# Kernel tuning notes

Measured on AMD Instinct MI355X. Metric: run time of the kernel, lower is better.

## Reference

```python
import jax, jax.numpy as jnp
import numpy as np

B, G, GS = 1024, 2000, 25   # batch, num gene groups, group size
H1, H2, C = 1024, 512, 10
EPS = 1e-5


def _xavier(key, shape, fan_in, fan_out):
    lim = np.sqrt(6.0 / (fan_in + fan_out))
    return jax.random.uniform(key, shape, jnp.float32, -lim, lim)


def setup_inputs() -> dict:
    key = jax.random.key(0)
    ks = jax.random.split(key, 8)
    x = jax.random.normal(ks[0], (B, G * GS), jnp.float32)
    # per-group Linear(GS, 1) weights stacked -> block-diagonal grouped GEMM
    gene_w = _xavier(ks[1], (G, GS), GS, 1)
    gene_b = jnp.zeros((G,), jnp.float32)
    W1 = _xavier(ks[2], (G, H1), G, H1)
    b1 = jnp.zeros((H1,), jnp.float32)
    W2 = _xavier(ks[3], (H1, H2), H1, H2)
    b2 = jnp.zeros((H2,), jnp.float32)
    Wout = _xavier(ks[4], (H2, C), H2, C)
    bout = jnp.zeros((C,), jnp.float32)
    Wres = _xavier(ks[5], (G, C), G, C)
    bres = jnp.zeros((C,), jnp.float32)
    gamma1 = jnp.ones((H1,), jnp.float32); beta1 = jnp.zeros((H1,), jnp.float32)
    gamma2 = jnp.ones((H2,), jnp.float32); beta2 = jnp.zeros((H2,), jnp.float32)
    return dict(x=x, gene_w=gene_w, gene_b=gene_b, W1=W1, b1=b1,
                gamma1=gamma1, beta1=beta1, W2=W2, b2=b2,
                gamma2=gamma2, beta2=beta2, Wout=Wout, bout=bout,
                Wres=Wres, bres=bres)


def _batch_norm(h, gamma, beta):
    # training-mode BatchNorm1d: biased batch statistics over axis 0
    mu = jnp.mean(h, axis=0)
    var = jnp.mean(jnp.square(h - mu), axis=0)
    return gamma * (h - mu) * jax.lax.rsqrt(var + EPS) + beta


def reference(x, gene_w, gene_b, W1, b1, gamma1, beta1, W2, b2,
              gamma2, beta2, Wout, bout, Wres, bres):
    # fused replacement for the per-group Linear(GS,1)+ReLU loop + cat
    xg = x.reshape(B, G, GS)
    g = jax.nn.relu(jnp.einsum('bgk,gk->bg', xg, gene_w) + gene_b)  # [B, G]
    h1 = jax.nn.relu(_batch_norm(g @ W1 + b1, gamma1, beta1))       # [B, H1]
    h2 = jax.nn.relu(_batch_norm(h1 @ W2 + b2, gamma2, beta2))      # [B, H2]
    x_main = h2 @ Wout + bout                                       # [B, C]
    x_res = g @ Wres + bres                                         # [B, C]
    return jax.nn.softmax(x_main + x_res, axis=1)
```

## Files before the change

kernel.cpp:

```cpp
#include <hip/hip_runtime.h>
#include <math.h>

#define NB   1024
#define NG   2000
#define NGS  25
#define KP   2048
#define NH1  1024
#define NH2  512
#define NC   10
#define EPSV 1e-5f
#define GPB  200

typedef __attribute__((ext_vector_type(8))) __bf16 bf16x8;
typedef __attribute__((ext_vector_type(4))) float f32x4;
typedef __attribute__((ext_vector_type(8))) unsigned short u16x8;
typedef __attribute__((ext_vector_type(4))) unsigned short u16x4;

__device__ __forceinline__ unsigned short f2bf(float f) {
  union { float f; unsigned u; } v; v.f = f;
  return (unsigned short)((v.u + 0x7fffu + ((v.u >> 16) & 1u)) >> 16);
}
__device__ __forceinline__ float bf2f(unsigned short b) {
  union { unsigned u; float f; } v; v.u = ((unsigned)b) << 16;
  return v.f;
}

__global__ __launch_bounds__(256) void gene_kernel(
    const float* __restrict__ x, const float* __restrict__ gw,
    const float* __restrict__ gb, unsigned short* __restrict__ g_bf) {
  __shared__ float xs[GPB * NGS];
  int b = blockIdx.x;
  int blk = blockIdx.y;
  const float4* src = (const float4*)(x + (size_t)b * (NG * NGS) + blk * (GPB * NGS));
  float4* dst = (float4*)xs;
  for (int i = threadIdx.x; i < (GPB * NGS) / 4; i += 256) dst[i] = src[i];
  __syncthreads();
  int j = threadIdx.x;
  if (j < GPB) {
    int gi = blk * GPB + j;
    const float* wp = gw + gi * NGS;
    const float* xp = xs + j * NGS;
    float acc = 0.f;
#pragma unroll
    for (int k = 0; k < NGS; ++k) acc = fmaf(xp[k], wp[k], acc);
    acc += gb[gi];
    g_bf[(size_t)b * KP + gi] = f2bf(fmaxf(acc, 0.f));
  } else if (blk == (NG / GPB - 1) && j < GPB + (KP - NG)) {
    g_bf[(size_t)b * KP + NG + (j - GPB)] = 0;
  }
}

__global__ __launch_bounds__(256) void convT_kernel(
    const float* __restrict__ src, unsigned short* __restrict__ dst,
    int K, int N, int Kpad) {
  __shared__ unsigned short ts[64][72];
  int k0 = blockIdx.x * 64, n0 = blockIdx.y * 64;
  int t = threadIdx.x;
  int c4 = (t & 15) * 4;
  int r  = t >> 4;
  for (int rr = r; rr < 64; rr += 16) {
    int k = k0 + rr;
    float4 v = make_float4(0.f, 0.f, 0.f, 0.f);
    if (k < K) v = *(const float4*)&src[(size_t)k * N + n0 + c4];
    ts[rr][c4 + 0] = f2bf(v.x); ts[rr][c4 + 1] = f2bf(v.y);
    ts[rr][c4 + 2] = f2bf(v.z); ts[rr][c4 + 3] = f2bf(v.w);
  }
  __syncthreads();
  int rr8 = (t & 7) * 8;
  int cc  = t >> 3;
  for (int c = cc; c < 64; c += 32) {
    u16x8 val;
#pragma unroll
    for (int i = 0; i < 8; ++i) val[i] = ts[rr8 + i][c];
    *(u16x8*)&dst[(size_t)(n0 + c) * Kpad + k0 + rr8] = val;
  }
}

__global__ __launch_bounds__(256) void gemm_bf16(
    const unsigned short* __restrict__ A,
    const unsigned short* __restrict__ Bt,
    float* __restrict__ C, int M, int N, int Kp) {
  __shared__ unsigned short As[64][72];
  __shared__ unsigned short Bs[64][72];
  int t = threadIdx.x;
  int m0 = blockIdx.y * 64, n0 = blockIdx.x * 64;
  int wave = t >> 6, lane = t & 63;
  int wm = (wave >> 1) * 32, wn = (wave & 1) * 32;
  int fm = lane & 15;
  int fk = (lane >> 4) * 8;

  int srow = t >> 3;
  int skc  = (t & 7) * 8;

  f32x4 acc[2][2];
#pragma unroll
  for (int i = 0; i < 2; ++i)
#pragma unroll
    for (int j = 0; j < 2; ++j) acc[i][j] = (f32x4){0.f, 0.f, 0.f, 0.f};

  const unsigned short* Ap = A + (size_t)(m0 + srow) * Kp + skc;
  const unsigned short* Bp = Bt + (size_t)(n0 + srow) * Kp + skc;
  size_t rstep = 32 * (size_t)Kp;

  u16x8 pa0 = *(const u16x8*)(Ap);
  u16x8 pa1 = *(const u16x8*)(Ap + rstep);
  u16x8 pb0 = *(const u16x8*)(Bp);
  u16x8 pb1 = *(const u16x8*)(Bp + rstep);

  for (int k0 = 0; k0 < Kp; k0 += 64) {
    *(u16x8*)&As[srow][skc]      = pa0;
    *(u16x8*)&As[srow + 32][skc] = pa1;
    *(u16x8*)&Bs[srow][skc]      = pb0;
    *(u16x8*)&Bs[srow + 32][skc] = pb1;
    __syncthreads();
    if (k0 + 64 < Kp) {
      pa0 = *(const u16x8*)(Ap + k0 + 64);
      pa1 = *(const u16x8*)(Ap + k0 + 64 + rstep);
      pb0 = *(const u16x8*)(Bp + k0 + 64);
      pb1 = *(const u16x8*)(Bp + k0 + 64 + rstep);
    }
#pragma unroll
    for (int s = 0; s < 2; ++s) {
      bf16x8 af[2], bfr[2];
      af[0]  = *(const bf16x8*)&As[wm + fm][s * 32 + fk];
      af[1]  = *(const bf16x8*)&As[wm + 16 + fm][s * 32 + fk];
      bfr[0] = *(const bf16x8*)&Bs[wn + fm][s * 32 + fk];
      bfr[1] = *(const bf16x8*)&Bs[wn + 16 + fm][s * 32 + fk];
#pragma unroll
      for (int i = 0; i < 2; ++i)
#pragma unroll
        for (int j = 0; j < 2; ++j)
          acc[i][j] = __builtin_amdgcn_mfma_f32_16x16x32_bf16(
              af[i], bfr[j], acc[i][j], 0, 0, 0);
    }
    __syncthreads();
  }

  int crow = (lane >> 4) * 4;
  int ccol = lane & 15;
#pragma unroll
  for (int i = 0; i < 2; ++i)
#pragma unroll
    for (int j = 0; j < 2; ++j)
#pragma unroll
      for (int r = 0; r < 4; ++r) {
        int m = m0 + wm + i * 16 + crow + r;
        int n = n0 + wn + j * 16 + ccol;
        C[(size_t)m * N + n] = acc[i][j][r];
      }
}

__global__ __launch_bounds__(256) void bn_stats(
    const float* __restrict__ t, float* __restrict__ sum,
    float* __restrict__ sq, int N) {
  int c  = blockIdx.x * blockDim.x + threadIdx.x;
  int r0 = blockIdx.y * 64;
  float s = 0.f, ss = 0.f;
  for (int r = r0; r < r0 + 64; ++r) {
    float v = t[(size_t)r * N + c];
    s += v;
    ss = fmaf(v, v, ss);
  }
  atomicAdd(&sum[c], s);
  atomicAdd(&sq[c], ss);
}

__global__ __launch_bounds__(256) void bn_apply_bf16(
    const float* __restrict__ t, unsigned short* __restrict__ o,
    const float* __restrict__ sum, const float* __restrict__ sq,
    const float* __restrict__ gamma, const float* __restrict__ beta,
    int nmask) {
  int idx = (blockIdx.x * 256 + threadIdx.x) * 4;
  float4 v = *(const float4*)&t[idx];
  float vv[4] = {v.x, v.y, v.z, v.w};
  u16x4 ov;
#pragma unroll
  for (int i = 0; i < 4; ++i) {
    int c = (idx + i) & nmask;
    float mu  = sum[c] * (1.f / NB);
    float var = sq[c] * (1.f / NB) - mu * mu;
    float h = (vv[i] - mu) * rsqrtf(var + EPSV);
    ov[i] = f2bf(fmaxf(fmaf(gamma[c], h, beta[c]), 0.f));
  }
  *(u16x4*)&o[idx] = ov;
}

__global__ __launch_bounds__(256) void bn_apply_f32(
    float* __restrict__ t, const float* __restrict__ sum,
    const float* __restrict__ sq, const float* __restrict__ gamma,
    const float* __restrict__ beta, int nmask) {
  int idx = (blockIdx.x * 256 + threadIdx.x) * 4;
  float4 v = *(const float4*)&t[idx];
  float vv[4] = {v.x, v.y, v.z, v.w};
#pragma unroll
  for (int i = 0; i < 4; ++i) {
    int c = (idx + i) & nmask;
    float mu  = sum[c] * (1.f / NB);
    float var = sq[c] * (1.f / NB) - mu * mu;
    float h = (vv[i] - mu) * rsqrtf(var + EPSV);
    vv[i] = fmaxf(fmaf(gamma[c], h, beta[c]), 0.f);
  }
  *(float4*)&t[idx] = make_float4(vv[0], vv[1], vv[2], vv[3]);
}

__global__ __launch_bounds__(256) void final_kernel(
    const float* __restrict__ h2, const unsigned short* __restrict__ g_bf,
    const float* __restrict__ Wout, const float* __restrict__ bout,
    const float* __restrict__ Wres, const float* __restrict__ bres,
    float* __restrict__ out) {
  int b = blockIdx.x;
  int t = threadIdx.x;
  float acc[NC] = {};

  if (t < NH2 / 4) {
    float4 hv = *(const float4*)&h2[(size_t)b * NH2 + t * 4];
    float hr[4] = {hv.x, hv.y, hv.z, hv.w};
    const float4* wp = (const float4*)&Wout[t * 4 * NC];
    float w[40];
#pragma unroll
    for (int q = 0; q < 10; ++q) {
      float4 wv = wp[q];
      w[q * 4] = wv.x; w[q * 4 + 1] = wv.y; w[q * 4 + 2] = wv.z; w[q * 4 + 3] = wv.w;
    }
#pragma unroll
    for (int r = 0; r < 4; ++r)
#pragma unroll
      for (int c = 0; c < NC; ++c) acc[c] = fmaf(hr[r], w[r * NC + c], acc[c]);
  }

  for (int u = t; u < NG / 4; u += 256) {
    u16x4 gv = *(const u16x4*)&g_bf[(size_t)b * KP + u * 4];
    float gr[4] = {bf2f(gv[0]), bf2f(gv[1]), bf2f(gv[2]), bf2f(gv[3])};
    const float4* wp = (const float4*)&Wres[u * 4 * NC];
    float w[40];
#pragma unroll
    for (int q = 0; q < 10; ++q) {
      float4 wv = wp[q];
      w[q * 4] = wv.x; w[q * 4 + 1] = wv.y; w[q * 4 + 2] = wv.z; w[q * 4 + 3] = wv.w;
    }
#pragma unroll
    for (int r = 0; r < 4; ++r)
#pragma unroll
      for (int c = 0; c < NC; ++c) acc[c] = fmaf(gr[r], w[r * NC + c], acc[c]);
  }

  __shared__ float red[4][NC];
  __shared__ float logits[NC];
  int lane = t & 63, wave = t >> 6;
#pragma unroll
  for (int c = 0; c < NC; ++c) {
    float v = acc[c];
    for (int off = 32; off > 0; off >>= 1) v += __shfl_down(v, off, 64);
    if (lane == 0) red[wave][c] = v;
  }
  __syncthreads();
  if (t < NC)
    logits[t] = red[0][t] + red[1][t] + red[2][t] + red[3][t] + bout[t] + bres[t];
  __syncthreads();
  if (t == 0) {
    float mx = logits[0];
#pragma unroll
    for (int c = 1; c < NC; ++c) mx = fmaxf(mx, logits[c]);
    float e[NC], s = 0.f;
#pragma unroll
    for (int c = 0; c < NC; ++c) { e[c] = expf(logits[c] - mx); s += e[c]; }
    float inv = 1.f / s;
#pragma unroll
    for (int c = 0; c < NC; ++c) out[(size_t)b * NC + c] = e[c] * inv;
  }
}

extern "C" void kernel_launch(void* const* d_in, const int* in_sizes, int n_in,
                              void* d_out, int out_size, void* d_ws, size_t ws_size,
                              hipStream_t stream) {
  const float* x      = (const float*)d_in[0];
  const float* gw     = (const float*)d_in[1];
  const float* gb     = (const float*)d_in[2];
  const float* W1     = (const float*)d_in[3];
  const float* gamma1 = (const float*)d_in[5];
  const float* beta1  = (const float*)d_in[6];
  const float* W2     = (const float*)d_in[7];
  const float* gamma2 = (const float*)d_in[9];
  const float* beta2  = (const float*)d_in[10];
  const float* Wout   = (const float*)d_in[11];
  const float* bout   = (const float*)d_in[12];
  const float* Wres   = (const float*)d_in[13];
  const float* bres   = (const float*)d_in[14];
  float* out = (float*)d_out;

  char* p = (char*)d_ws;
  unsigned short* g_bf  = (unsigned short*)p; p += (size_t)NB * KP * 2;
  unsigned short* W1bT  = (unsigned short*)p; p += (size_t)NH1 * KP * 2;
  unsigned short* W2bT  = (unsigned short*)p; p += (size_t)NH2 * NH1 * 2;
  float* t1  = (float*)p; p += (size_t)NB * NH1 * 4;
  unsigned short* t1b = (unsigned short*)p; p += (size_t)NB * NH1 * 2;
  float* t2  = (float*)p; p += (size_t)NB * NH2 * 4;
  float* stats = (float*)p;
  float* sum1 = stats, *sq1 = stats + 1024, *sum2 = stats + 2048, *sq2 = stats + 2560;

  hipMemsetAsync(stats, 0, 3072 * sizeof(float), stream);

  convT_kernel<<<dim3(KP / 64, NH1 / 64), 256, 0, stream>>>(W1, W1bT, NG, NH1, KP);
  convT_kernel<<<dim3(NH1 / 64, NH2 / 64), 256, 0, stream>>>(W2, W2bT, NH1, NH2, NH1);

  gene_kernel<<<dim3(NB, NG / GPB), 256, 0, stream>>>(x, gw, gb, g_bf);

  gemm_bf16<<<dim3(NH1 / 64, NB / 64), 256, 0, stream>>>(g_bf, W1bT, t1, NB, NH1, KP);
  bn_stats<<<dim3(NH1 / 256, 16), 256, 0, stream>>>(t1, sum1, sq1, NH1);
  bn_apply_bf16<<<(NB * NH1 / 4) / 256, 256, 0, stream>>>(t1, t1b, sum1, sq1,
                                                          gamma1, beta1, NH1 - 1);

  gemm_bf16<<<dim3(NH2 / 64, NB / 64), 256, 0, stream>>>(t1b, W2bT, t2, NB, NH2, NH1);
  bn_stats<<<dim3(NH2 / 256, 16), 256, 0, stream>>>(t2, sum2, sq2, NH2);
  bn_apply_f32<<<(NB * NH2 / 4) / 256, 256, 0, stream>>>(t2, sum2, sq2,
                                                         gamma2, beta2, NH2 - 1);

  final_kernel<<<NB, 256, 0, stream>>>(t2, g_bf, Wout, bout, Wres, bres, out);
}
```

Baseline: 386.0 us.

## Fuse BatchNorm stats into GEMM epilogues and BN apply into consumer loads

BatchNorm column statistics are now accumulated in the GEMM epilogues via wave shuffles and atomics, which removes the separate bn_stats passes. BN1 apply plus ReLU plus the bf16 cast moves into the A-tile load of the second GEMM, and BN2 apply moves into the final kernel. The two weight-transpose launches are merged into one grid. This removes several full-tensor read/write passes and kernel launches, at the cost of extra per-tile normalization math and fp32 A loads in GEMM2.

```diff
diff --git a/kernel.cpp b/kernel.cpp
--- a/kernel.cpp
+++ b/kernel.cpp
@@ -50,9 +50,15 @@
   }
 }
 
-__global__ __launch_bounds__(256) void convT_kernel(
-    const float* __restrict__ src, unsigned short* __restrict__ dst,
-    int K, int N, int Kpad) {
+__global__ __launch_bounds__(256) void convT_dual(
+    const float* __restrict__ W1, unsigned short* __restrict__ W1bT,
+    const float* __restrict__ W2, unsigned short* __restrict__ W2bT) {
+  const float* src; unsigned short* dst; int K, N, Kpad;
+  if (blockIdx.z == 0) { src = W1; dst = W1bT; K = NG; N = NH1; Kpad = KP; }
+  else {
+    src = W2; dst = W2bT; K = NH1; N = NH2; Kpad = NH1;
+    if (blockIdx.x >= NH1 / 64 || blockIdx.y >= NH2 / 64) return;
+  }
   __shared__ unsigned short ts[64][72];
   int k0 = blockIdx.x * 64, n0 = blockIdx.y * 64;
   int t = threadIdx.x;
@@ -76,21 +82,19 @@
   }
 }
 
-__global__ __launch_bounds__(256) void gemm_bf16(
+__global__ __launch_bounds__(256) void gemm1_kernel(
     const unsigned short* __restrict__ A,
     const unsigned short* __restrict__ Bt,
-    float* __restrict__ C, int M, int N, int Kp) {
+    float* __restrict__ C, float* __restrict__ sum, float* __restrict__ sq,
+    int M, int N, int Kp) {
   __shared__ unsigned short As[64][72];
   __shared__ unsigned short Bs[64][72];
   int t = threadIdx.x;
   int m0 = blockIdx.y * 64, n0 = blockIdx.x * 64;
   int wave = t >> 6, lane = t & 63;
   int wm = (wave >> 1) * 32, wn = (wave & 1) * 32;
-  int fm = lane & 15;
-  int fk = (lane >> 4) * 8;
-
-  int srow = t >> 3;
-  int skc  = (t & 7) * 8;
+  int fm = lane & 15, fk = (lane >> 4) * 8;
+  int srow = t >> 3, skc = (t & 7) * 8;
 
   f32x4 acc[2][2];
 #pragma unroll
@@ -136,75 +140,142 @@
     __syncthreads();
   }
 
-  int crow = (lane >> 4) * 4;
-  int ccol = lane & 15;
-#pragma unroll
-  for (int i = 0; i < 2; ++i)
-#pragma unroll
-    for (int j = 0; j < 2; ++j)
+  int crow = (lane >> 4) * 4, ccol = lane & 15;
+#pragma unroll
+  for (int j = 0; j < 2; ++j) {
+    float s = 0.f, ss = 0.f;
+#pragma unroll
+    for (int i = 0; i < 2; ++i)
 #pragma unroll
       for (int r = 0; r < 4; ++r) {
+        float v = acc[i][j][r];
         int m = m0 + wm + i * 16 + crow + r;
         int n = n0 + wn + j * 16 + ccol;
-        C[(size_t)m * N + n] = acc[i][j][r];
+        C[(size_t)m * N + n] = v;
+        s += v;
+        ss = fmaf(v, v, ss);
       }
-}
-
-__global__ __launch_bounds__(256) void bn_stats(
-    const float* __restrict__ t, float* __restrict__ sum,
-    float* __restrict__ sq, int N) {
-  int c  = blockIdx.x * blockDim.x + threadIdx.x;
-  int r0 = blockIdx.y * 64;
-  float s = 0.f, ss = 0.f;
-  for (int r = r0; r < r0 + 64; ++r) {
-    float v = t[(size_t)r * N + c];
-    s += v;
-    ss = fmaf(v, v, ss);
-  }
-  atomicAdd(&sum[c], s);
-  atomicAdd(&sq[c], ss);
-}
-
-__global__ __launch_bounds__(256) void bn_apply_bf16(
-    const float* __restrict__ t, unsigned short* __restrict__ o,
-    const float* __restrict__ sum, const float* __restrict__ sq,
-    const float* __restrict__ gamma, const float* __restrict__ beta,
-    int nmask) {
-  int idx = (blockIdx.x * 256 + threadIdx.x) * 4;
-  float4 v = *(const float4*)&t[idx];
-  float vv[4] = {v.x, v.y, v.z, v.w};
-  u16x4 ov;
-#pragma unroll
-  for (int i = 0; i < 4; ++i) {
-    int c = (idx + i) & nmask;
-    float mu  = sum[c] * (1.f / NB);
-    float var = sq[c] * (1.f / NB) - mu * mu;
-    float h = (vv[i] - mu) * rsqrtf(var + EPSV);
-    ov[i] = f2bf(fmaxf(fmaf(gamma[c], h, beta[c]), 0.f));
-  }
-  *(u16x4*)&o[idx] = ov;
-}
-
-__global__ __launch_bounds__(256) void bn_apply_f32(
-    float* __restrict__ t, const float* __restrict__ sum,
-    const float* __restrict__ sq, const float* __restrict__ gamma,
-    const float* __restrict__ beta, int nmask) {
-  int idx = (blockIdx.x * 256 + threadIdx.x) * 4;
-  float4 v = *(const float4*)&t[idx];
-  float vv[4] = {v.x, v.y, v.z, v.w};
-#pragma unroll
-  for (int i = 0; i < 4; ++i) {
-    int c = (idx + i) & nmask;
-    float mu  = sum[c] * (1.f / NB);
-    float var = sq[c] * (1.f / NB) - mu * mu;
-    float h = (vv[i] - mu) * rsqrtf(var + EPSV);
-    vv[i] = fmaxf(fmaf(gamma[c], h, beta[c]), 0.f);
-  }
-  *(float4*)&t[idx] = make_float4(vv[0], vv[1], vv[2], vv[3]);
+    s  += __shfl_down(s, 32, 64);  s  += __shfl_down(s, 16, 64);
+    ss += __shfl_down(ss, 32, 64); ss += __shfl_down(ss, 16, 64);
+    if (lane < 16) {
+      atomicAdd(&sum[n0 + wn + j * 16 + lane], s);
+      atomicAdd(&sq[n0 + wn + j * 16 + lane], ss);
+    }
+  }
+}
+
+__global__ __launch_bounds__(256) void gemm2_kernel(
+    const float* __restrict__ A,
+    const unsigned short* __restrict__ Bt,
+    float* __restrict__ C, const float* __restrict__ sum1,
+    const float* __restrict__ sq1, const float* __restrict__ gam1,
+    const float* __restrict__ bet1, float* __restrict__ sum2,
+    float* __restrict__ sq2, int M, int N, int Kp) {
+  __shared__ unsigned short As[64][72];
+  __shared__ unsigned short Bs[64][72];
+  int t = threadIdx.x;
+  int m0 = blockIdx.y * 64, n0 = blockIdx.x * 64;
+  int wave = t >> 6, lane = t & 63;
+  int wm = (wave >> 1) * 32, wn = (wave & 1) * 32;
+  int fm = lane & 15, fk = (lane >> 4) * 8;
+  int srow = t >> 3, skc = (t & 7) * 8;
+
+  f32x4 acc[2][2];
+#pragma unroll
+  for (int i = 0; i < 2; ++i)
+#pragma unroll
+    for (int j = 0; j < 2; ++j) acc[i][j] = (f32x4){0.f, 0.f, 0.f, 0.f};
+
+  const float* Ap = A + (size_t)(m0 + srow) * Kp + skc;
+  const unsigned short* Bp = Bt + (size_t)(n0 + srow) * Kp + skc;
+  size_t rstepA = 32 * (size_t)Kp;
+  size_t rstepB = 32 * (size_t)Kp;
+
+  f32x4 pa[4];
+  pa[0] = *(const f32x4*)(Ap);
+  pa[1] = *(const f32x4*)(Ap + 4);
+  pa[2] = *(const f32x4*)(Ap + rstepA);
+  pa[3] = *(const f32x4*)(Ap + rstepA + 4);
+  u16x8 pb0 = *(const u16x8*)(Bp);
+  u16x8 pb1 = *(const u16x8*)(Bp + rstepB);
+
+  for (int k0 = 0; k0 < Kp; k0 += 64) {
+    float sc[8], sh[8];
+#pragma unroll
+    for (int i = 0; i < 8; ++i) {
+      int k = k0 + skc + i;
+      float mu  = sum1[k] * (1.f / NB);
+      float var = sq1[k] * (1.f / NB) - mu * mu;
+      float rs  = rsqrtf(var + EPSV);
+      sc[i] = gam1[k] * rs;
+      sh[i] = fmaf(-mu, sc[i], bet1[k]);
+    }
+    u16x8 a0, a1;
+#pragma unroll
+    for (int i = 0; i < 4; ++i) {
+      a0[i]     = f2bf(fmaxf(fmaf(pa[0][i], sc[i],     sh[i]),     0.f));
+      a0[i + 4] = f2bf(fmaxf(fmaf(pa[1][i], sc[i + 4], sh[i + 4]), 0.f));
+      a1[i]     = f2bf(fmaxf(fmaf(pa[2][i], sc[i],     sh[i]),     0.f));
+      a1[i + 4] = f2bf(fmaxf(fmaf(pa[3][i], sc[i + 4], sh[i + 4]), 0.f));
+    }
+    *(u16x8*)&As[srow][skc]      = a0;
+    *(u16x8*)&As[srow + 32][skc] = a1;
+    *(u16x8*)&Bs[srow][skc]      = pb0;
+    *(u16x8*)&Bs[srow + 32][skc] = pb1;
+    __syncthreads();
+    if (k0 + 64 < Kp) {
+      pa[0] = *(const f32x4*)(Ap + k0 + 64);
+      pa[1] = *(const f32x4*)(Ap + k0 + 64 + 4);
+      pa[2] = *(const f32x4*)(Ap + k0 + 64 + rstepA);
+      pa[3] = *(const f32x4*)(Ap + k0 + 64 + rstepA + 4);
+      pb0 = *(const u16x8*)(Bp + k0 + 64);
+      pb1 = *(const u16x8*)(Bp + k0 + 64 + rstepB);
+    }
+#pragma unroll
+    for (int s = 0; s < 2; ++s) {
+      bf16x8 af[2], bfr[2];
+      af[0]  = *(const bf16x8*)&As[wm + fm][s * 32 + fk];
+      af[1]  = *(const bf16x8*)&As[wm + 16 + fm][s * 32 + fk];
+      bfr[0] = *(const bf16x8*)&Bs[wn + fm][s * 32 + fk];
+      bfr[1] = *(const bf16x8*)&Bs[wn + 16 + fm][s * 32 + fk];
+#pragma unroll
+      for (int i = 0; i < 2; ++i)
+#pragma unroll
+        for (int j = 0; j < 2; ++j)
+          acc[i][j] = __builtin_amdgcn_mfma_f32_16x16x32_bf16(
+              af[i], bfr[j], acc[i][j], 0, 0, 0);
+    }
+    __syncthreads();
+  }
+
+  int crow = (lane >> 4) * 4, ccol = lane & 15;
+#pragma unroll
+  for (int j = 0; j < 2; ++j) {
+    float s = 0.f, ss = 0.f;
+#pragma unroll
+    for (int i = 0; i < 2; ++i)
+#pragma unroll
+      for (int r = 0; r < 4; ++r) {
+        float v = acc[i][j][r];
+        int m = m0 + wm + i * 16 + crow + r;
+        int n = n0 + wn + j * 16 + ccol;
+        C[(size_t)m * N + n] = v;
+        s += v;
+        ss = fmaf(v, v, ss);
+      }
+    s  += __shfl_down(s, 32, 64);  s  += __shfl_down(s, 16, 64);
+    ss += __shfl_down(ss, 32, 64); ss += __shfl_down(ss, 16, 64);
+    if (lane < 16) {
+      atomicAdd(&sum2[n0 + wn + j * 16 + lane], s);
+      atomicAdd(&sq2[n0 + wn + j * 16 + lane], ss);
+    }
+  }
 }
 
 __global__ __launch_bounds__(256) void final_kernel(
-    const float* __restrict__ h2, const unsigned short* __restrict__ g_bf,
+    const float* __restrict__ t2, const float* __restrict__ sum2,
+    const float* __restrict__ sq2, const float* __restrict__ gam2,
+    const float* __restrict__ bet2, const unsigned short* __restrict__ g_bf,
     const float* __restrict__ Wout, const float* __restrict__ bout,
     const float* __restrict__ Wres, const float* __restrict__ bres,
     float* __restrict__ out) {
@@ -213,8 +284,18 @@
   float acc[NC] = {};
 
   if (t < NH2 / 4) {
-    float4 hv = *(const float4*)&h2[(size_t)b * NH2 + t * 4];
-    float hr[4] = {hv.x, hv.y, hv.z, hv.w};
+    float4 tv = *(const float4*)&t2[(size_t)b * NH2 + t * 4];
+    float raw[4] = {tv.x, tv.y, tv.z, tv.w};
+    float hr[4];
+#pragma unroll
+    for (int i = 0; i < 4; ++i) {
+      int c = t * 4 + i;
+      float mu  = sum2[c] * (1.f / NB);
+      float var = sq2[c] * (1.f / NB) - mu * mu;
+      float rs  = rsqrtf(var + EPSV);
+      float scv = gam2[c] * rs;
+      hr[i] = fmaxf(fmaf(raw[i], scv, fmaf(-mu, scv, bet2[c])), 0.f);
+    }
     const float4* wp = (const float4*)&Wout[t * 4 * NC];
     float w[40];
 #pragma unroll
@@ -289,31 +370,26 @@
   float* out = (float*)d_out;
 
   char* p = (char*)d_ws;
-  unsigned short* g_bf  = (unsigned short*)p; p += (size_t)NB * KP * 2;
-  unsigned short* W1bT  = (unsigned short*)p; p += (size_t)NH1 * KP * 2;
-  unsigned short* W2bT  = (unsigned short*)p; p += (size_t)NH2 * NH1 * 2;
-  float* t1  = (float*)p; p += (size_t)NB * NH1 * 4;
-  unsigned short* t1b = (unsigned short*)p; p += (size_t)NB * NH1 * 2;
-  float* t2  = (float*)p; p += (size_t)NB * NH2 * 4;
+  unsigned short* g_bf = (unsigned short*)p; p += (size_t)NB * KP * 2;
+  unsigned short* W1bT = (unsigned short*)p; p += (size_t)NH1 * KP * 2;
+  unsigned short* W2bT = (unsigned short*)p; p += (size_t)NH2 * NH1 * 2;
+  float* t1 = (float*)p; p += (size_t)NB * NH1 * 4;
+  float* t2 = (float*)p; p += (size_t)NB * NH2 * 4;
   float* stats = (float*)p;
   float* sum1 = stats, *sq1 = stats + 1024, *sum2 = stats + 2048, *sq2 = stats + 2560;
 
   hipMemsetAsync(stats, 0, 3072 * sizeof(float), stream);
 
-  convT_kernel<<<dim3(KP / 64, NH1 / 64), 256, 0, stream>>>(W1, W1bT, NG, NH1, KP);
-  convT_kernel<<<dim3(NH1 / 64, NH2 / 64), 256, 0, stream>>>(W2, W2bT, NH1, NH2, NH1);
+  convT_dual<<<dim3(KP / 64, NH1 / 64, 2), 256, 0, stream>>>(W1, W1bT, W2, W2bT);
 
   gene_kernel<<<dim3(NB, NG / GPB), 256, 0, stream>>>(x, gw, gb, g_bf);
 
-  gemm_bf16<<<dim3(NH1 / 64, NB / 64), 256, 0, stream>>>(g_bf, W1bT, t1, NB, NH1, KP);
-  bn_stats<<<dim3(NH1 / 256, 16), 256, 0, stream>>>(t1, sum1, sq1, NH1);
-  bn_apply_bf16<<<(NB * NH1 / 4) / 256, 256, 0, stream>>>(t1, t1b, sum1, sq1,
-                                                          gamma1, beta1, NH1 - 1);
-
-  gemm_bf16<<<dim3(NH2 / 64, NB / 64), 256, 0, stream>>>(t1b, W2bT, t2, NB, NH2, NH1);
-  bn_stats<<<dim3(NH2 / 256, 16), 256, 0, stream>>>(t2, sum2, sq2, NH2);
-  bn_apply_f32<<<(NB * NH2 / 4) / 256, 256, 0, stream>>>(t2, sum2, sq2,
-                                                         gamma2, beta2, NH2 - 1);
-
-  final_kernel<<<NB, 256, 0, stream>>>(t2, g_bf, Wout, bout, Wres, bres, out);
-}
+  gemm1_kernel<<<dim3(NH1 / 64, NB / 64), 256, 0, stream>>>(
+      g_bf, W1bT, t1, sum1, sq1, NB, NH1, KP);
+
+  gemm2_kernel<<<dim3(NH2 / 64, NB / 64), 256, 0, stream>>>(
+      t1, W2bT, t2, sum1, sq1, gamma1, beta1, sum2, sq2, NB, NH2, NH1);
+
+  final_kernel<<<NB, 256, 0, stream>>>(t2, sum2, sq2, gamma2, beta2, g_bf,
+                                       Wout, bout, Wres, bres, out);
+}
```

Result: faster. 372.5 us (-3.5%).
